# Kernel tuning notes

Measured on AMD Instinct MI355X. Metric: run time of the kernel, lower is better.

Reference implementation:

```python
import jax, jax.numpy as jnp
import numpy as np

B, T, D, E, H = 4, 2048, 2048, 4, 8192  # H = 4*D
TOPK = 2
CAPACITY_FACTOR = 1


def setup_inputs() -> dict:
    key = jax.random.key(0)
    k0, k1, k2, k3 = jax.random.split(key, 4)
    x = jax.random.normal(k0, (B, T, D), dtype=jnp.float32)
    Wg = jax.random.normal(k1, (D, E), dtype=jnp.float32) * 0.02  # router gate weight
    bg = jnp.zeros((E,), dtype=jnp.float32)                        # router gate bias (nn.Linear default)
    W1 = jax.random.normal(k2, (E, D, H), dtype=jnp.float32) * (1.0 / np.sqrt(D))  # per-expert fc (no bias)
    W2 = jax.random.normal(k3, (E, H, D), dtype=jnp.float32) * (1.0 / np.sqrt(H))  # per-expert proj (no bias)
    return {"x": x, "Wg": Wg, "bg": bg, "W1": W1, "W2": W2}


def reference(x, Wg, bg, W1, W2):
    Bq, Tq, Dq = x.shape
    N = Bq * Tq
    capacity = int(N * CAPACITY_FACTOR / E)  # static python int

    flat_x = x.reshape(N, Dq)
    logits = flat_x @ Wg + bg                              # [N, E]
    top_vals, top_idx = jax.lax.top_k(logits, TOPK)        # [N, TOPK]
    sparse = jnp.full_like(logits, -jnp.inf)
    sparse = sparse.at[jnp.arange(N)[:, None], top_idx].set(top_vals)
    probs = jax.nn.softmax(sparse, axis=-1)                # zeros outside top-k

    out = jnp.zeros_like(flat_x)
    for i in range(E):  # small fixed expert count
        assigned = (top_idx == i).any(axis=-1)             # [N]
        score = jnp.where(assigned, probs[:, i], -jnp.inf)
        sel_p, sel_idx = jax.lax.top_k(score, capacity)    # capacity-limited, highest prob first
        p = jnp.where(jnp.isfinite(sel_p), sel_p, 0.0)[:, None]  # invalid slots contribute 0
        tok = flat_x[sel_idx]                              # [cap, D]
        h = jax.nn.gelu(tok @ W1[i], approximate=False)    # exact GELU like nn.GELU()
        y = (h @ W2[i]) * p                                # [cap, D]
        out = out.at[sel_idx].add(y)
    return out.reshape(Bq, Tq, Dq)
```

## Files before the change

kernel.cpp:

```cpp
#include <hip/hip_runtime.h>
#include <hip/hip_bf16.h>
#include <math.h>
#include <stdint.h>

#define N_TOK 8192
#define DMODEL 2048
#define NEXP 4
#define HDIM 8192
#define CAP 2048

typedef __attribute__((ext_vector_type(4))) float f32x4;
typedef __attribute__((ext_vector_type(8))) short s16x8;
typedef __attribute__((ext_vector_type(4))) unsigned short u16x4;

__device__ __forceinline__ unsigned short f2bf(float f) {
  __hip_bfloat16 h = __float2bfloat16(f);
  return __builtin_bit_cast(unsigned short, h);
}

__device__ __forceinline__ void gload_lds16(const void* g, void* l) {
  __builtin_amdgcn_global_load_lds(
      (const __attribute__((address_space(1))) unsigned int*)(uintptr_t)g,
      (__attribute__((address_space(3))) unsigned int*)(unsigned int)(uintptr_t)l,
      16, 0, 0);
}

__global__ __launch_bounds__(256) void router_kernel(
    const float* __restrict__ x, const float* __restrict__ Wg,
    const float* __restrict__ bg, unsigned long long* __restrict__ keys) {
  int token = blockIdx.x * 4 + (threadIdx.x >> 6);
  int lane = threadIdx.x & 63;
  const float* xr = x + (size_t)token * DMODEL;
  double a0 = 0, a1 = 0, a2 = 0, a3 = 0;
  for (int i = lane; i < DMODEL; i += 64) {
    float xv = xr[i];
    float4 w = ((const float4*)Wg)[i];
    a0 += (double)xv * (double)w.x;
    a1 += (double)xv * (double)w.y;
    a2 += (double)xv * (double)w.z;
    a3 += (double)xv * (double)w.w;
  }
  for (int off = 32; off > 0; off >>= 1) {
    a0 += __shfl_down(a0, off);
    a1 += __shfl_down(a1, off);
    a2 += __shfl_down(a2, off);
    a3 += __shfl_down(a3, off);
  }
  if (lane == 0) {
    float l[4] = {(float)(a0 + (double)bg[0]), (float)(a1 + (double)bg[1]),
                  (float)(a2 + (double)bg[2]), (float)(a3 + (double)bg[3])};
    int e1 = 0;
    for (int e = 1; e < 4; ++e) if (l[e] > l[e1]) e1 = e;
    int e2 = (e1 == 0) ? 1 : 0;
    for (int e = e2 + 1; e < 4; ++e) { if (e == e1) continue; if (l[e] > l[e2]) e2 = e; }
    float d = l[e2] - l[e1];
    float ex = expf(d);
    float z = 1.0f + ex;
    float p1 = 1.0f / z, p2 = ex / z;
    unsigned lo = 0xFFFFFFFFu - (unsigned)token;
    for (int e = 0; e < 4; ++e) {
      unsigned hi = (e == e1) ? __float_as_uint(p1) : (e == e2) ? __float_as_uint(p2) : 0u;
      keys[(size_t)e * N_TOK + token] = ((unsigned long long)hi << 32) | lo;
    }
  }
}

__global__ __launch_bounds__(256) void rank_select_kernel(
    const unsigned long long* __restrict__ keys, int* __restrict__ sel_idx,
    float* __restrict__ sel_p) {
  __shared__ unsigned long long kbuf[2048];
  const int e = blockIdx.y;
  const int i = blockIdx.x * 256 + threadIdx.x;
  const unsigned long long my = keys[(size_t)e * N_TOK + i];
  int rank = 0;
  for (int c = 0; c < N_TOK; c += 2048) {
    __syncthreads();
    for (int j = threadIdx.x; j < 2048; j += 256)
      kbuf[j] = keys[(size_t)e * N_TOK + c + j];
    __syncthreads();
#pragma unroll 8
    for (int j = 0; j < 2048; j += 2) {
      unsigned long long k0 = kbuf[j], k1 = kbuf[j + 1];
      rank += (k0 > my) + (k1 > my);
    }
  }
  if (rank < CAP) {
    sel_idx[e * CAP + rank] = i;
    sel_p[e * CAP + rank] = __uint_as_float((unsigned)(my >> 32));
  }
}

__global__ __launch_bounds__(256) void gather_kernel(
    const float* __restrict__ x, const int* __restrict__ sel_idx,
    unsigned short* __restrict__ tok) {
  int row = blockIdx.x;
  int t = sel_idx[row];
  const float4* src = (const float4*)(x + (size_t)t * DMODEL);
  u16x4* dst = (u16x4*)(tok + (size_t)row * DMODEL);
  for (int i = threadIdx.x; i < DMODEL / 4; i += blockDim.x) {
    float4 v = src[i];
    u16x4 w = {f2bf(v.x), f2bf(v.y), f2bf(v.z), f2bf(v.w)};
    dst[i] = w;
  }
}

__global__ __launch_bounds__(256) void transpose_convert_kernel(
    const float* __restrict__ W, unsigned short* __restrict__ WT, int K, int N) {
  __shared__ unsigned short tile[64][68];
  const size_t eoff = (size_t)blockIdx.z * (size_t)K * N;
  const float* Wp = W + eoff;
  unsigned short* Tp = WT + eoff;
  const int n0 = blockIdx.x * 64, k0 = blockIdx.y * 64;
  const int tid = threadIdx.x;
  const int nn4 = tid & 15, kk = tid >> 4;
#pragma unroll
  for (int p = 0; p < 4; ++p) {
    int k = kk + p * 16;
    float4 v = *(const float4*)&Wp[(size_t)(k0 + k) * N + n0 + nn4 * 4];
    tile[nn4 * 4 + 0][k] = f2bf(v.x);
    tile[nn4 * 4 + 1][k] = f2bf(v.y);
    tile[nn4 * 4 + 2][k] = f2bf(v.z);
    tile[nn4 * 4 + 3][k] = f2bf(v.w);
  }
  __syncthreads();
  const int nw = tid >> 4, cw = (tid & 15) * 4;
#pragma unroll
  for (int p = 0; p < 4; ++p) {
    int n = nw + p * 16;
    u16x4 v = *(const u16x4*)&tile[n][cw];
    *(u16x4*)&Tp[(size_t)(n0 + n) * K + k0 + cw] = v;
  }
}

template <int EPI>
__global__ __launch_bounds__(512) void gemm_kernel(
    const unsigned short* __restrict__ A, const unsigned short* __restrict__ Bt,
    void* __restrict__ C, const int* __restrict__ sel_idx, const float* __restrict__ sel_p,
    int M, int N, int K, size_t b_stride) {
  __shared__ unsigned short sh[73728];
  const int tid = threadIdx.x;
  const int lane = tid & 63;
  const int w = tid >> 6;
  const int wm = w >> 1, wn = w & 1;

  const int nwg = gridDim.x * gridDim.y;
  const int cpx = nwg >> 3;
  int linear = blockIdx.y * gridDim.x + blockIdx.x;
  linear = (linear & 7) * cpx + (linear >> 3);
  const int bx = linear & (gridDim.x - 1);
  const int by = linear >> __builtin_ctz(gridDim.x);
  const int m0 = by * 256, n0 = bx * 128;
  const unsigned short* Bp = Bt + (size_t)(m0 >> 11) * b_stride;

  f32x4 acc[4][4];
#pragma unroll
  for (int i = 0; i < 4; ++i)
#pragma unroll
    for (int j = 0; j < 4; ++j) acc[i][j] = (f32x4){0.f, 0.f, 0.f, 0.f};

  const int srow = tid >> 3;
  const int schunk = ((tid & 7) ^ (srow & 7)) * 8;
  const unsigned short* gA = A + (size_t)(m0 + srow) * K + schunk;
  const unsigned short* gB = Bp + (size_t)(n0 + srow) * K + schunk;

  const int csw0 = (((lane >> 4) ^ (lane & 7)) << 3);
  const int arow = wm * 64 + (lane & 15);
  const int brow = wn * 64 + (lane & 15);

#define STAGE_A(buf, i, kt) \
  gload_lds16(gA + (size_t)((i) * 64) * K + (kt), &sh[(buf) * 24576 + ((i) * 64 + w * 8) * 64])
#define STAGE_B(buf, i, kt) \
  gload_lds16(gB + (size_t)((i) * 64) * K + (kt), &sh[(buf) * 24576 + 16384 + ((i) * 64 + w * 8) * 64])

  STAGE_A(0, 0, 0); STAGE_A(0, 1, 0); STAGE_A(0, 2, 0); STAGE_A(0, 3, 0);
  STAGE_B(0, 0, 0); STAGE_B(0, 1, 0);
  STAGE_A(1, 0, 64); STAGE_A(1, 1, 64); STAGE_A(1, 2, 64); STAGE_A(1, 3, 64);
  STAGE_B(1, 0, 64); STAGE_B(1, 1, 64);
  asm volatile("s_waitcnt vmcnt(6)" ::: "memory");
  __builtin_amdgcn_s_barrier();

  const int NT = K >> 6;
  int buf = 0, pbuf = 2;
  for (int t = 0; t < NT; ++t) {
    const unsigned short* shA = &sh[buf * 24576];
    const unsigned short* shB = &sh[buf * 24576 + 16384];
    const bool pf = (t + 2) < NT;
    const int pkt = (t + 2) << 6;
    if (pf) { STAGE_A(pbuf, 0, pkt); STAGE_A(pbuf, 1, pkt); STAGE_A(pbuf, 2, pkt); }
    {
      s16x8 av[4], bv[4];
#pragma unroll
      for (int mf = 0; mf < 4; ++mf) av[mf] = *(const s16x8*)&shA[(arow + mf * 16) * 64 + csw0];
#pragma unroll
      for (int nf = 0; nf < 4; ++nf) bv[nf] = *(const s16x8*)&shB[(brow + nf * 16) * 64 + csw0];
      __builtin_amdgcn_s_setprio(1);
#pragma unroll
      for (int mf = 0; mf < 4; ++mf)
#pragma unroll
        for (int nf = 0; nf < 4; ++nf)
          acc[mf][nf] = __builtin_amdgcn_mfma_f32_16x16x32_bf16(av[mf], bv[nf], acc[mf][nf], 0, 0, 0);
      __builtin_amdgcn_s_setprio(0);
    }
    if (pf) { STAGE_A(pbuf, 3, pkt); STAGE_B(pbuf, 0, pkt); STAGE_B(pbuf, 1, pkt); }
    {
      const int csw1 = csw0 ^ 32;
      s16x8 av[4], bv[4];
#pragma unroll
      for (int mf = 0; mf < 4; ++mf) av[mf] = *(const s16x8*)&shA[(arow + mf * 16) * 64 + csw1];
#pragma unroll
      for (int nf = 0; nf < 4; ++nf) bv[nf] = *(const s16x8*)&shB[(brow + nf * 16) * 64 + csw1];
      __builtin_amdgcn_s_setprio(1);
#pragma unroll
      for (int mf = 0; mf < 4; ++mf)
#pragma unroll
        for (int nf = 0; nf < 4; ++nf)
          acc[mf][nf] = __builtin_amdgcn_mfma_f32_16x16x32_bf16(av[mf], bv[nf], acc[mf][nf], 0, 0, 0);
      __builtin_amdgcn_s_setprio(0);
    }
    if (pf) {
      asm volatile("s_waitcnt vmcnt(6)" ::: "memory");
    } else {
      asm volatile("s_waitcnt vmcnt(0)" ::: "memory");
    }
    __builtin_amdgcn_s_barrier();
    buf = (buf == 2) ? 0 : buf + 1;
    pbuf = (pbuf == 2) ? 0 : pbuf + 1;
  }
#undef STAGE_A
#undef STAGE_B

  if (EPI == 0) {
    unsigned short* Hc = (unsigned short*)C;
#pragma unroll
    for (int mf = 0; mf < 4; ++mf) {
      int rowb = m0 + wm * 64 + mf * 16 + ((lane >> 4) << 2);
#pragma unroll
      for (int nf = 0; nf < 4; ++nf) {
        int col = n0 + wn * 64 + nf * 16 + (lane & 15);
#pragma unroll
        for (int r = 0; r < 4; ++r) {
          float v = acc[mf][nf][r];
          float g = 0.5f * v * (1.0f + erff(v * 0.70710678118654752f));
          Hc[(size_t)(rowb + r) * N + col] = f2bf(g);
        }
      }
    }
  } else {
    float* O = (float*)C;
#pragma unroll
    for (int mf = 0; mf < 4; ++mf) {
      int rowb = m0 + wm * 64 + mf * 16 + ((lane >> 4) << 2);
      int tk[4];
      float pv[4];
#pragma unroll
      for (int r = 0; r < 4; ++r) { tk[r] = sel_idx[rowb + r]; pv[r] = sel_p[rowb + r]; }
#pragma unroll
      for (int nf = 0; nf < 4; ++nf) {
        int col = n0 + wn * 64 + nf * 16 + (lane & 15);
#pragma unroll
        for (int r = 0; r < 4; ++r)
          atomicAdd(&O[(size_t)tk[r] * DMODEL + col], acc[mf][nf][r] * pv[r]);
      }
    }
  }
}

extern "C" void kernel_launch(void* const* d_in, const int* in_sizes, int n_in,
                              void* d_out, int out_size, void* d_ws, size_t ws_size,
                              hipStream_t stream) {
  const float* x  = (const float*)d_in[0];
  const float* Wg = (const float*)d_in[1];
  const float* bg = (const float*)d_in[2];
  const float* W1 = (const float*)d_in[3];
  const float* W2 = (const float*)d_in[4];
  float* out = (float*)d_out;

  char* ws = (char*)d_ws;
  unsigned long long* keys = (unsigned long long*)ws;
  int*   sel_idx = (int*)(ws + 262144);
  float* sel_p   = (float*)(ws + 262144 + 32768);
  unsigned short* tok = (unsigned short*)(ws + 327680);
  const size_t tok_b = (size_t)N_TOK * DMODEL * 2;
  const size_t h_b   = (size_t)N_TOK * HDIM * 2;
  const size_t w_b   = (size_t)NEXP * DMODEL * HDIM * 2;
  const size_t base  = 327680 + tok_b;

  hipMemsetAsync(d_out, 0, (size_t)out_size * sizeof(float), stream);
  router_kernel<<<N_TOK / 4, 256, 0, stream>>>(x, Wg, bg, keys);
  rank_select_kernel<<<dim3(N_TOK / 256, NEXP), 256, 0, stream>>>(keys, sel_idx, sel_p);
  gather_kernel<<<NEXP * CAP, 256, 0, stream>>>(x, sel_idx, tok);

  if (ws_size >= base + h_b + 2 * w_b) {
    unsigned short* h   = (unsigned short*)(ws + base);
    unsigned short* W1T = (unsigned short*)(ws + base + h_b);
    unsigned short* W2T = (unsigned short*)(ws + base + h_b + w_b);
    transpose_convert_kernel<<<dim3(HDIM / 64, DMODEL / 64, NEXP), 256, 0, stream>>>(
        W1, W1T, DMODEL, HDIM);
    transpose_convert_kernel<<<dim3(DMODEL / 64, HDIM / 64, NEXP), 256, 0, stream>>>(
        W2, W2T, HDIM, DMODEL);
    gemm_kernel<0><<<dim3(HDIM / 128, N_TOK / 256), 512, 0, stream>>>(
        tok, W1T, h, nullptr, nullptr, N_TOK, HDIM, DMODEL, (size_t)DMODEL * HDIM);
    gemm_kernel<1><<<dim3(DMODEL / 128, N_TOK / 256), 512, 0, stream>>>(
        h, W2T, out, sel_idx, sel_p, N_TOK, DMODEL, HDIM, (size_t)DMODEL * HDIM);
  } else {
    unsigned short* h    = (unsigned short*)(ws + base);
    unsigned short* wbuf = (unsigned short*)(ws + base + (size_t)CAP * HDIM * 2);
    for (int e = 0; e < NEXP; ++e) {
      transpose_convert_kernel<<<dim3(HDIM / 64, DMODEL / 64, 1), 256, 0, stream>>>(
          W1 + (size_t)e * DMODEL * HDIM, wbuf, DMODEL, HDIM);
      gemm_kernel<0><<<dim3(HDIM / 128, CAP / 256), 512, 0, stream>>>(
          tok + (size_t)e * CAP * DMODEL, wbuf, h, nullptr, nullptr, CAP, HDIM, DMODEL, 0);
      transpose_convert_kernel<<<dim3(DMODEL / 64, HDIM / 64, 1), 256, 0, stream>>>(
          W2 + (size_t)e * HDIM * DMODEL, wbuf, HDIM, DMODEL);
      gemm_kernel<1><<<dim3(DMODEL / 128, CAP / 256), 512, 0, stream>>>(
          h, wbuf, out, sel_idx + e * CAP, sel_p + e * CAP, CAP, DMODEL, HDIM, 0);
    }
  }
}
```

Baseline: 896.3 us.

## Enlarge GEMM tile to 256x256 with BK=32 four-stage LDS pipeline

Both expert GEMMs now use 256x256 output tiles per workgroup instead of 256x128, with 8 waves arranged 2x4 and each wave computing 128x64. The K step shrinks from 64 to 32 and the pipeline moves to four LDS slots with three tiles in flight, along with a new XOR swizzle and split prefetch placement. The aim is to raise arithmetic intensity and cut global and LDS traffic per FLOP. In exchange, accumulator register pressure doubles and the grid holds half as many workgroups, which may hurt occupancy and load balance across CUs.

```diff
diff --git a/kernel.cpp b/kernel.cpp
--- a/kernel.cpp
+++ b/kernel.cpp
@@ -137,11 +137,11 @@
     const unsigned short* __restrict__ A, const unsigned short* __restrict__ Bt,
     void* __restrict__ C, const int* __restrict__ sel_idx, const float* __restrict__ sel_p,
     int M, int N, int K, size_t b_stride) {
-  __shared__ unsigned short sh[73728];
+  __shared__ unsigned short sh[65536];
   const int tid = threadIdx.x;
   const int lane = tid & 63;
   const int w = tid >> 6;
-  const int wm = w >> 1, wn = w & 1;
+  const int wm = w >> 2, wn = w & 3;
 
   const int nwg = gridDim.x * gridDim.y;
   const int cpx = nwg >> 3;
@@ -149,91 +149,102 @@
   linear = (linear & 7) * cpx + (linear >> 3);
   const int bx = linear & (gridDim.x - 1);
   const int by = linear >> __builtin_ctz(gridDim.x);
-  const int m0 = by * 256, n0 = bx * 128;
+  const int m0 = by * 256, n0 = bx * 256;
   const unsigned short* Bp = Bt + (size_t)(m0 >> 11) * b_stride;
 
-  f32x4 acc[4][4];
-#pragma unroll
-  for (int i = 0; i < 4; ++i)
+  f32x4 acc[8][4];
+#pragma unroll
+  for (int i = 0; i < 8; ++i)
 #pragma unroll
     for (int j = 0; j < 4; ++j) acc[i][j] = (f32x4){0.f, 0.f, 0.f, 0.f};
 
-  const int srow = tid >> 3;
-  const int schunk = ((tid & 7) ^ (srow & 7)) * 8;
-  const unsigned short* gA = A + (size_t)(m0 + srow) * K + schunk;
-  const unsigned short* gB = Bp + (size_t)(n0 + srow) * K + schunk;
-
-  const int csw0 = (((lane >> 4) ^ (lane & 7)) << 3);
-  const int arow = wm * 64 + (lane & 15);
+  const int srow = (lane >> 2);
+  const int schunk = ((lane & 3) ^ ((lane >> 3) & 3)) * 8;
+  const unsigned short* gA0 = A + (size_t)(m0 + w * 16 + srow) * K + schunk;
+  const unsigned short* gA1 = gA0 + (size_t)128 * K;
+  const unsigned short* gB0 = Bp + (size_t)(n0 + w * 16 + srow) * K + schunk;
+  const unsigned short* gB1 = gB0 + (size_t)128 * K;
+  const int ldsA0 = (w * 16) * 32;
+  const int ldsA1 = (128 + w * 16) * 32;
+  const int ldsB0 = 8192 + (w * 16) * 32;
+  const int ldsB1 = 8192 + (128 + w * 16) * 32;
+
+  const int koff = (((lane >> 4) ^ ((lane >> 1) & 3)) << 3);
+  const int arow = wm * 128 + (lane & 15);
   const int brow = wn * 64 + (lane & 15);
 
-#define STAGE_A(buf, i, kt) \
-  gload_lds16(gA + (size_t)((i) * 64) * K + (kt), &sh[(buf) * 24576 + ((i) * 64 + w * 8) * 64])
-#define STAGE_B(buf, i, kt) \
-  gload_lds16(gB + (size_t)((i) * 64) * K + (kt), &sh[(buf) * 24576 + 16384 + ((i) * 64 + w * 8) * 64])
-
-  STAGE_A(0, 0, 0); STAGE_A(0, 1, 0); STAGE_A(0, 2, 0); STAGE_A(0, 3, 0);
-  STAGE_B(0, 0, 0); STAGE_B(0, 1, 0);
-  STAGE_A(1, 0, 64); STAGE_A(1, 1, 64); STAGE_A(1, 2, 64); STAGE_A(1, 3, 64);
-  STAGE_B(1, 0, 64); STAGE_B(1, 1, 64);
-  asm volatile("s_waitcnt vmcnt(6)" ::: "memory");
+#define STAGE_AH(slot, kt) do { \
+    gload_lds16(gA0 + (kt), &sh[(slot) * 16384 + ldsA0]); \
+    gload_lds16(gA1 + (kt), &sh[(slot) * 16384 + ldsA1]); } while (0)
+#define STAGE_BH(slot, kt) do { \
+    gload_lds16(gB0 + (kt), &sh[(slot) * 16384 + ldsB0]); \
+    gload_lds16(gB1 + (kt), &sh[(slot) * 16384 + ldsB1]); } while (0)
+
+#define COMPUTE_TILE(slot) do { \
+    const unsigned short* shA = &sh[(slot) * 16384]; \
+    const unsigned short* shB = shA + 8192; \
+    s16x8 av[4], bv[4]; \
+    _Pragma("unroll") \
+    for (int nf = 0; nf < 4; ++nf) bv[nf] = *(const s16x8*)&shB[(brow + nf * 16) * 32 + koff]; \
+    _Pragma("unroll") \
+    for (int mf = 0; mf < 4; ++mf) av[mf] = *(const s16x8*)&shA[(arow + mf * 16) * 32 + koff]; \
+    __builtin_amdgcn_s_setprio(1); \
+    _Pragma("unroll") \
+    for (int mf = 0; mf < 4; ++mf) \
+      _Pragma("unroll") \
+      for (int nf = 0; nf < 4; ++nf) \
+        acc[mf][nf] = __builtin_amdgcn_mfma_f32_16x16x32_bf16(av[mf], bv[nf], acc[mf][nf], 0, 0, 0); \
+    __builtin_amdgcn_s_setprio(0); \
+    PF_B \
+    _Pragma("unroll") \
+    for (int mf = 0; mf < 4; ++mf) av[mf] = *(const s16x8*)&shA[(arow + 64 + mf * 16) * 32 + koff]; \
+    __builtin_amdgcn_s_setprio(1); \
+    _Pragma("unroll") \
+    for (int mf = 0; mf < 4; ++mf) \
+      _Pragma("unroll") \
+      for (int nf = 0; nf < 4; ++nf) \
+        acc[4 + mf][nf] = __builtin_amdgcn_mfma_f32_16x16x32_bf16(av[mf], bv[nf], acc[4 + mf][nf], 0, 0, 0); \
+    __builtin_amdgcn_s_setprio(0); \
+  } while (0)
+
+  STAGE_AH(0, 0); STAGE_BH(0, 0);
+  STAGE_AH(1, 32); STAGE_BH(1, 32);
+  STAGE_AH(2, 64); STAGE_BH(2, 64);
+  asm volatile("s_waitcnt vmcnt(8)" ::: "memory");
   __builtin_amdgcn_s_barrier();
 
-  const int NT = K >> 6;
-  int buf = 0, pbuf = 2;
-  for (int t = 0; t < NT; ++t) {
-    const unsigned short* shA = &sh[buf * 24576];
-    const unsigned short* shB = &sh[buf * 24576 + 16384];
-    const bool pf = (t + 2) < NT;
-    const int pkt = (t + 2) << 6;
-    if (pf) { STAGE_A(pbuf, 0, pkt); STAGE_A(pbuf, 1, pkt); STAGE_A(pbuf, 2, pkt); }
-    {
-      s16x8 av[4], bv[4];
-#pragma unroll
-      for (int mf = 0; mf < 4; ++mf) av[mf] = *(const s16x8*)&shA[(arow + mf * 16) * 64 + csw0];
-#pragma unroll
-      for (int nf = 0; nf < 4; ++nf) bv[nf] = *(const s16x8*)&shB[(brow + nf * 16) * 64 + csw0];
-      __builtin_amdgcn_s_setprio(1);
-#pragma unroll
-      for (int mf = 0; mf < 4; ++mf)
-#pragma unroll
-        for (int nf = 0; nf < 4; ++nf)
-          acc[mf][nf] = __builtin_amdgcn_mfma_f32_16x16x32_bf16(av[mf], bv[nf], acc[mf][nf], 0, 0, 0);
-      __builtin_amdgcn_s_setprio(0);
-    }
-    if (pf) { STAGE_A(pbuf, 3, pkt); STAGE_B(pbuf, 0, pkt); STAGE_B(pbuf, 1, pkt); }
-    {
-      const int csw1 = csw0 ^ 32;
-      s16x8 av[4], bv[4];
-#pragma unroll
-      for (int mf = 0; mf < 4; ++mf) av[mf] = *(const s16x8*)&shA[(arow + mf * 16) * 64 + csw1];
-#pragma unroll
-      for (int nf = 0; nf < 4; ++nf) bv[nf] = *(const s16x8*)&shB[(brow + nf * 16) * 64 + csw1];
-      __builtin_amdgcn_s_setprio(1);
-#pragma unroll
-      for (int mf = 0; mf < 4; ++mf)
-#pragma unroll
-        for (int nf = 0; nf < 4; ++nf)
-          acc[mf][nf] = __builtin_amdgcn_mfma_f32_16x16x32_bf16(av[mf], bv[nf], acc[mf][nf], 0, 0, 0);
-      __builtin_amdgcn_s_setprio(0);
-    }
-    if (pf) {
-      asm volatile("s_waitcnt vmcnt(6)" ::: "memory");
-    } else {
-      asm volatile("s_waitcnt vmcnt(0)" ::: "memory");
-    }
+  const int NT = K >> 5;
+  int t = 0;
+  for (; t + 3 < NT; ++t) {
+    const int slot = t & 3, psl = (t + 3) & 3;
+    const int pkt = (t + 3) << 5;
+    STAGE_AH(psl, pkt);
+#define PF_B STAGE_BH(psl, pkt);
+    COMPUTE_TILE(slot);
+#undef PF_B
+    asm volatile("s_waitcnt vmcnt(8)" ::: "memory");
     __builtin_amdgcn_s_barrier();
-    buf = (buf == 2) ? 0 : buf + 1;
-    pbuf = (pbuf == 2) ? 0 : pbuf + 1;
-  }
-#undef STAGE_A
-#undef STAGE_B
+  }
+#define PF_B
+  COMPUTE_TILE(t & 3);
+  asm volatile("s_waitcnt vmcnt(4)" ::: "memory");
+  __builtin_amdgcn_s_barrier();
+  ++t;
+  COMPUTE_TILE(t & 3);
+  asm volatile("s_waitcnt vmcnt(0)" ::: "memory");
+  __builtin_amdgcn_s_barrier();
+  ++t;
+  COMPUTE_TILE(t & 3);
+#undef PF_B
+#undef COMPUTE_TILE
+#undef STAGE_AH
+#undef STAGE_BH
 
   if (EPI == 0) {
     unsigned short* Hc = (unsigned short*)C;
 #pragma unroll
-    for (int mf = 0; mf < 4; ++mf) {
-      int rowb = m0 + wm * 64 + mf * 16 + ((lane >> 4) << 2);
+    for (int mf = 0; mf < 8; ++mf) {
+      int rowb = m0 + wm * 128 + mf * 16 + ((lane >> 4) << 2);
 #pragma unroll
       for (int nf = 0; nf < 4; ++nf) {
         int col = n0 + wn * 64 + nf * 16 + (lane & 15);
@@ -248,8 +259,8 @@
   } else {
     float* O = (float*)C;
 #pragma unroll
-    for (int mf = 0; mf < 4; ++mf) {
-      int rowb = m0 + wm * 64 + mf * 16 + ((lane >> 4) << 2);
+    for (int mf = 0; mf < 8; ++mf) {
+      int rowb = m0 + wm * 128 + mf * 16 + ((lane >> 4) << 2);
       int tk[4];
       float pv[4];
 #pragma unroll
@@ -298,9 +309,9 @@
         W1, W1T, DMODEL, HDIM);
     transpose_convert_kernel<<<dim3(DMODEL / 64, HDIM / 64, NEXP), 256, 0, stream>>>(
         W2, W2T, HDIM, DMODEL);
-    gemm_kernel<0><<<dim3(HDIM / 128, N_TOK / 256), 512, 0, stream>>>(
+    gemm_kernel<0><<<dim3(HDIM / 256, N_TOK / 256), 512, 0, stream>>>(
         tok, W1T, h, nullptr, nullptr, N_TOK, HDIM, DMODEL, (size_t)DMODEL * HDIM);
-    gemm_kernel<1><<<dim3(DMODEL / 128, N_TOK / 256), 512, 0, stream>>>(
+    gemm_kernel<1><<<dim3(DMODEL / 256, N_TOK / 256), 512, 0, stream>>>(
         h, W2T, out, sel_idx, sel_p, N_TOK, DMODEL, HDIM, (size_t)DMODEL * HDIM);
   } else {
     unsigned short* h    = (unsigned short*)(ws + base);
@@ -308,11 +319,11 @@
     for (int e = 0; e < NEXP; ++e) {
       transpose_convert_kernel<<<dim3(HDIM / 64, DMODEL / 64, 1), 256, 0, stream>>>(
           W1 + (size_t)e * DMODEL * HDIM, wbuf, DMODEL, HDIM);
-      gemm_kernel<0><<<dim3(HDIM / 128, CAP / 256), 512, 0, stream>>>(
+      gemm_kernel<0><<<dim3(HDIM / 256, CAP / 256), 512, 0, stream>>>(
           tok + (size_t)e * CAP * DMODEL, wbuf, h, nullptr, nullptr, CAP, HDIM, DMODEL, 0);
       transpose_convert_kernel<<<dim3(DMODEL / 64, HDIM / 64, 1), 256, 0, stream>>>(
           W2 + (size_t)e * HDIM * DMODEL, wbuf, HDIM, DMODEL);
-      gemm_kernel<1><<<dim3(DMODEL / 128, CAP / 256), 512, 0, stream>>>(
+      gemm_kernel<1><<<dim3(DMODEL / 256, CAP / 256), 512, 0, stream>>>(
           h, wbuf, out, sel_idx + e * CAP, sel_p + e * CAP, CAP, DMODEL, HDIM, 0);
     }
   }
```

New measurement: 879.8 us. No clear change (-1.8%).

## Enlarge GEMM tile to 256x256 with a 4-stage K-32 LDS pipeline

Applied to the files above, without the earlier changes.

The expert GEMM block tile grows from 256x128 to 256x256, with waves arranged 2x4 and each wave computing 128x64 through an 8x4 accumulator array. The K loop now steps by 32 through a 4-slot LDS ring with 3-stage-ahead prefetch. Each K step is split into two MFMA phases separated by barriers and sched_barrier so that prefetches interleave with compute. The aim is higher arithmetic intensity per LDS and global load. In exchange, register pressure roughly doubles, there are more barriers per K step, and the grid shrinks to half as many workgroups.

```diff
diff --git a/kernel.cpp b/kernel.cpp
--- a/kernel.cpp
+++ b/kernel.cpp
@@ -137,11 +137,11 @@
     const unsigned short* __restrict__ A, const unsigned short* __restrict__ Bt,
     void* __restrict__ C, const int* __restrict__ sel_idx, const float* __restrict__ sel_p,
     int M, int N, int K, size_t b_stride) {
-  __shared__ unsigned short sh[73728];
+  __shared__ unsigned short sh[65536];
   const int tid = threadIdx.x;
   const int lane = tid & 63;
   const int w = tid >> 6;
-  const int wm = w >> 1, wn = w & 1;
+  const int wm = w >> 2, wn = w & 3;
 
   const int nwg = gridDim.x * gridDim.y;
   const int cpx = nwg >> 3;
@@ -149,91 +149,90 @@
   linear = (linear & 7) * cpx + (linear >> 3);
   const int bx = linear & (gridDim.x - 1);
   const int by = linear >> __builtin_ctz(gridDim.x);
-  const int m0 = by * 256, n0 = bx * 128;
+  const int m0 = by * 256, n0 = bx * 256;
   const unsigned short* Bp = Bt + (size_t)(m0 >> 11) * b_stride;
 
-  f32x4 acc[4][4];
-#pragma unroll
-  for (int i = 0; i < 4; ++i)
+  f32x4 acc[8][4];
+#pragma unroll
+  for (int i = 0; i < 8; ++i)
 #pragma unroll
     for (int j = 0; j < 4; ++j) acc[i][j] = (f32x4){0.f, 0.f, 0.f, 0.f};
 
-  const int srow = tid >> 3;
-  const int schunk = ((tid & 7) ^ (srow & 7)) * 8;
-  const unsigned short* gA = A + (size_t)(m0 + srow) * K + schunk;
-  const unsigned short* gB = Bp + (size_t)(n0 + srow) * K + schunk;
-
-  const int csw0 = (((lane >> 4) ^ (lane & 7)) << 3);
-  const int arow = wm * 64 + (lane & 15);
+  const unsigned short* gA = A + (size_t)(m0 + w * 16 + (lane >> 2)) * K + (lane & 3) * 8;
+  const unsigned short* gB = Bp + (size_t)(n0 + w * 16 + (lane >> 2)) * K + (lane & 3) * 8;
+  const int ldsSt = w * 512;
+
+#define STA(slot, j) do { \
+    gload_lds16(gA + (size_t)(j) * 32, &sh[(slot) * 8192 + ldsSt]); \
+    gload_lds16(gA + (size_t)128 * K + (size_t)(j) * 32, &sh[(slot) * 8192 + 4096 + ldsSt]); \
+  } while (0)
+#define STB(slot, j) do { \
+    gload_lds16(gB + (size_t)(j) * 32, &sh[32768 + (slot) * 8192 + ldsSt]); \
+    gload_lds16(gB + (size_t)128 * K + (size_t)(j) * 32, &sh[32768 + (slot) * 8192 + 4096 + ldsSt]); \
+  } while (0)
+
+  const int arow = wm * 128 + (lane & 15);
   const int brow = wn * 64 + (lane & 15);
-
-#define STAGE_A(buf, i, kt) \
-  gload_lds16(gA + (size_t)((i) * 64) * K + (kt), &sh[(buf) * 24576 + ((i) * 64 + w * 8) * 64])
-#define STAGE_B(buf, i, kt) \
-  gload_lds16(gB + (size_t)((i) * 64) * K + (kt), &sh[(buf) * 24576 + 16384 + ((i) * 64 + w * 8) * 64])
-
-  STAGE_A(0, 0, 0); STAGE_A(0, 1, 0); STAGE_A(0, 2, 0); STAGE_A(0, 3, 0);
-  STAGE_B(0, 0, 0); STAGE_B(0, 1, 0);
-  STAGE_A(1, 0, 64); STAGE_A(1, 1, 64); STAGE_A(1, 2, 64); STAGE_A(1, 3, 64);
-  STAGE_B(1, 0, 64); STAGE_B(1, 1, 64);
-  asm volatile("s_waitcnt vmcnt(6)" ::: "memory");
+  const int kc = (lane >> 4) * 8;
+
+  STA(0, 0); STB(0, 0);
+  STA(1, 1); STB(1, 1);
+  STA(2, 2); STB(2, 2);
+  asm volatile("s_waitcnt vmcnt(8)" ::: "memory");
   __builtin_amdgcn_s_barrier();
 
-  const int NT = K >> 6;
-  int buf = 0, pbuf = 2;
-  for (int t = 0; t < NT; ++t) {
-    const unsigned short* shA = &sh[buf * 24576];
-    const unsigned short* shB = &sh[buf * 24576 + 16384];
-    const bool pf = (t + 2) < NT;
-    const int pkt = (t + 2) << 6;
-    if (pf) { STAGE_A(pbuf, 0, pkt); STAGE_A(pbuf, 1, pkt); STAGE_A(pbuf, 2, pkt); }
-    {
-      s16x8 av[4], bv[4];
-#pragma unroll
-      for (int mf = 0; mf < 4; ++mf) av[mf] = *(const s16x8*)&shA[(arow + mf * 16) * 64 + csw0];
-#pragma unroll
-      for (int nf = 0; nf < 4; ++nf) bv[nf] = *(const s16x8*)&shB[(brow + nf * 16) * 64 + csw0];
-      __builtin_amdgcn_s_setprio(1);
-#pragma unroll
-      for (int mf = 0; mf < 4; ++mf)
-#pragma unroll
-        for (int nf = 0; nf < 4; ++nf)
-          acc[mf][nf] = __builtin_amdgcn_mfma_f32_16x16x32_bf16(av[mf], bv[nf], acc[mf][nf], 0, 0, 0);
-      __builtin_amdgcn_s_setprio(0);
-    }
-    if (pf) { STAGE_A(pbuf, 3, pkt); STAGE_B(pbuf, 0, pkt); STAGE_B(pbuf, 1, pkt); }
-    {
-      const int csw1 = csw0 ^ 32;
-      s16x8 av[4], bv[4];
-#pragma unroll
-      for (int mf = 0; mf < 4; ++mf) av[mf] = *(const s16x8*)&shA[(arow + mf * 16) * 64 + csw1];
-#pragma unroll
-      for (int nf = 0; nf < 4; ++nf) bv[nf] = *(const s16x8*)&shB[(brow + nf * 16) * 64 + csw1];
-      __builtin_amdgcn_s_setprio(1);
-#pragma unroll
-      for (int mf = 0; mf < 4; ++mf)
-#pragma unroll
-        for (int nf = 0; nf < 4; ++nf)
-          acc[mf][nf] = __builtin_amdgcn_mfma_f32_16x16x32_bf16(av[mf], bv[nf], acc[mf][nf], 0, 0, 0);
-      __builtin_amdgcn_s_setprio(0);
-    }
-    if (pf) {
-      asm volatile("s_waitcnt vmcnt(6)" ::: "memory");
-    } else {
-      asm volatile("s_waitcnt vmcnt(0)" ::: "memory");
-    }
+  const int NS = K >> 5;
+  for (int j = 0; j < NS; ++j) {
+    const unsigned short* sa = &sh[(j & 3) * 8192];
+    const unsigned short* sb = &sh[32768 + (j & 3) * 8192];
+    const bool pf = (j + 3) < NS;
+    const int psl = (j + 3) & 3;
+    s16x8 av[4], bv[4];
+#pragma unroll
+    for (int nf = 0; nf < 4; ++nf)
+      bv[nf] = *(const s16x8*)&sb[(brow + nf * 16) * 32 + kc];
+#pragma unroll
+    for (int mf = 0; mf < 4; ++mf)
+      av[mf] = *(const s16x8*)&sa[(arow + mf * 16) * 32 + kc];
+    if (pf) STA(psl, j + 3);
     __builtin_amdgcn_s_barrier();
-    buf = (buf == 2) ? 0 : buf + 1;
-    pbuf = (pbuf == 2) ? 0 : pbuf + 1;
-  }
-#undef STAGE_A
-#undef STAGE_B
+    asm volatile("s_waitcnt lgkmcnt(0)" ::: "memory");
+    __builtin_amdgcn_sched_barrier(0);
+    __builtin_amdgcn_s_setprio(1);
+#pragma unroll
+    for (int mf = 0; mf < 4; ++mf)
+#pragma unroll
+      for (int nf = 0; nf < 4; ++nf)
+        acc[mf][nf] = __builtin_amdgcn_mfma_f32_16x16x32_bf16(av[mf], bv[nf], acc[mf][nf], 0, 0, 0);
+    __builtin_amdgcn_s_setprio(0);
+    __builtin_amdgcn_s_barrier();
+#pragma unroll
+    for (int mf = 0; mf < 4; ++mf)
+      av[mf] = *(const s16x8*)&sa[(arow + 64 + mf * 16) * 32 + kc];
+    if (pf) STB(psl, j + 3);
+    if (pf)                   asm volatile("s_waitcnt vmcnt(8)" ::: "memory");
+    else if ((j + 2) < NS)    asm volatile("s_waitcnt vmcnt(4)" ::: "memory");
+    else                      asm volatile("s_waitcnt vmcnt(0)" ::: "memory");
+    __builtin_amdgcn_s_barrier();
+    asm volatile("s_waitcnt lgkmcnt(0)" ::: "memory");
+    __builtin_amdgcn_sched_barrier(0);
+    __builtin_amdgcn_s_setprio(1);
+#pragma unroll
+    for (int mf = 0; mf < 4; ++mf)
+#pragma unroll
+      for (int nf = 0; nf < 4; ++nf)
+        acc[4 + mf][nf] = __builtin_amdgcn_mfma_f32_16x16x32_bf16(av[mf], bv[nf], acc[4 + mf][nf], 0, 0, 0);
+    __builtin_amdgcn_s_setprio(0);
+    __builtin_amdgcn_s_barrier();
+  }
+#undef STA
+#undef STB
 
   if (EPI == 0) {
     unsigned short* Hc = (unsigned short*)C;
 #pragma unroll
-    for (int mf = 0; mf < 4; ++mf) {
-      int rowb = m0 + wm * 64 + mf * 16 + ((lane >> 4) << 2);
+    for (int mf = 0; mf < 8; ++mf) {
+      int rowb = m0 + wm * 128 + mf * 16 + ((lane >> 4) << 2);
 #pragma unroll
       for (int nf = 0; nf < 4; ++nf) {
         int col = n0 + wn * 64 + nf * 16 + (lane & 15);
@@ -248,8 +247,8 @@
   } else {
     float* O = (float*)C;
 #pragma unroll
-    for (int mf = 0; mf < 4; ++mf) {
-      int rowb = m0 + wm * 64 + mf * 16 + ((lane >> 4) << 2);
+    for (int mf = 0; mf < 8; ++mf) {
+      int rowb = m0 + wm * 128 + mf * 16 + ((lane >> 4) << 2);
       int tk[4];
       float pv[4];
 #pragma unroll
@@ -298,9 +297,9 @@
         W1, W1T, DMODEL, HDIM);
     transpose_convert_kernel<<<dim3(DMODEL / 64, HDIM / 64, NEXP), 256, 0, stream>>>(
         W2, W2T, HDIM, DMODEL);
-    gemm_kernel<0><<<dim3(HDIM / 128, N_TOK / 256), 512, 0, stream>>>(
+    gemm_kernel<0><<<dim3(HDIM / 256, N_TOK / 256), 512, 0, stream>>>(
         tok, W1T, h, nullptr, nullptr, N_TOK, HDIM, DMODEL, (size_t)DMODEL * HDIM);
-    gemm_kernel<1><<<dim3(DMODEL / 128, N_TOK / 256), 512, 0, stream>>>(
+    gemm_kernel<1><<<dim3(DMODEL / 256, N_TOK / 256), 512, 0, stream>>>(
         h, W2T, out, sel_idx, sel_p, N_TOK, DMODEL, HDIM, (size_t)DMODEL * HDIM);
   } else {
     unsigned short* h    = (unsigned short*)(ws + base);
@@ -308,11 +307,11 @@
     for (int e = 0; e < NEXP; ++e) {
       transpose_convert_kernel<<<dim3(HDIM / 64, DMODEL / 64, 1), 256, 0, stream>>>(
           W1 + (size_t)e * DMODEL * HDIM, wbuf, DMODEL, HDIM);
-      gemm_kernel<0><<<dim3(HDIM / 128, CAP / 256), 512, 0, stream>>>(
+      gemm_kernel<0><<<dim3(HDIM / 256, CAP / 256), 512, 0, stream>>>(
           tok + (size_t)e * CAP * DMODEL, wbuf, h, nullptr, nullptr, CAP, HDIM, DMODEL, 0);
       transpose_convert_kernel<<<dim3(DMODEL / 64, HDIM / 64, 1), 256, 0, stream>>>(
           W2 + (size_t)e * HDIM * DMODEL, wbuf, HDIM, DMODEL);
-      gemm_kernel<1><<<dim3(DMODEL / 128, CAP / 256), 512, 0, stream>>>(
+      gemm_kernel<1><<<dim3(DMODEL / 256, CAP / 256), 512, 0, stream>>>(
           h, wbuf, out, sel_idx + e * CAP, sel_p + e * CAP, CAP, DMODEL, HDIM, 0);
     }
   }
```

After: 909.3 us. About the same (+1.5%).
